# Optimization experiments

Measured on AMD Instinct MI355X. Metric: run time of the kernel, lower is better.

## Reference

```python
import jax, jax.numpy as jnp
import numpy as np

T = 8        # n_segment
T_OUT = 8    # t_out
G = 4        # n_group
K = 3        # correlation_neighbor


def setup_inputs() -> dict:
    key = jax.random.key(0)
    k1, k2, k3 = jax.random.split(key, 3)
    x = jax.random.normal(k1, (64, 256, 56, 56), dtype=jnp.float32)
    # grouped 1x1 conv: in=G*(T-1)*K*K=252 (63 per group), out=T_OUT*G*T=256 (64 per group)
    conv_w = jax.random.normal(k2, (G, T_OUT * T, (T - 1) * K * K), dtype=jnp.float32) * 0.05
    conv_b = jax.random.normal(k3, (G, T_OUT * T), dtype=jnp.float32) * 0.05
    return {"x": x, "conv_w": conv_w, "conv_b": conv_b}


def reference(x, conv_w, conv_b):
    nt, c, h, w = x.shape
    nb = nt // T
    cpg = c // G
    pad = K // 2

    x5 = x.reshape(nb, T, c, h, w)
    # ReplicationPad2d(pad) on spatial dims
    xp = jnp.pad(x5, ((0, 0), (0, 0), (0, 0), (pad, pad), (pad, pad)), mode='edge')

    # 9-way shifted cost volume: per-group channel-sum of x[t] * x_pad[t+1] shifted
    a = x5[:, :T - 1].reshape(nb, T - 1, G, cpg, h, w)
    corr_list = []
    for i in range(K):
        for j in range(K):
            b = xp[:, 1:, :, i:i + h, j:j + w].reshape(nb, T - 1, G, cpg, h, w)
            corr_list.append(jnp.einsum('ntgchw,ntgchw->ntghw', a, b))
    corr = jnp.stack(corr_list, axis=3)                     # (nb, T-1, G, K*K, h, w)
    corr = corr.transpose(0, 2, 1, 3, 4, 5)                 # (nb, G, T-1, K*K, h, w)
    corr = corr.reshape(nb, G, (T - 1) * K * K, h, w)

    # grouped 1x1 conv
    wx = jnp.einsum('ngihw,goi->ngohw', corr, conv_w) + conv_b[None, :, :, None, None]
    wx = wx.reshape(nb, G, T_OUT, T, h, w).transpose(2, 1, 0, 3, 4, 5)  # (t_out, G, nb, T, h, w)

    # torch splits c as (c_per_group, G) here (c_per_group outer) — mimic exactly
    xs = x5.reshape(nb, T, cpg, G, h, w).transpose(2, 3, 0, 1, 4, 5)   # (cpg, G, nb, T, h, w)

    # weighted segment-sum over T for each output frame
    xsum = jnp.einsum('ognthw,cgnthw->ocgnhw', wx, xs)      # (t_out, cpg, G, nb, h, w)

    # residual: x at frame floor(i*T/t_out)
    i_in = (np.arange(T_OUT) * T) // T_OUT
    res = xs[:, :, :, i_in].transpose(3, 0, 1, 2, 4, 5)     # (t_out, cpg, G, nb, h, w)

    out = (xsum + res).transpose(3, 0, 2, 1, 4, 5)          # (nb, t_out, G, cpg, h, w)
    return out.reshape(nb * T_OUT, c, h, w)
```

## Files before the change

kernel.cpp:

```cpp
#include <hip/hip_runtime.h>

namespace {
constexpr int NBb = 8;
constexpr int TT  = 8;
constexpr int TOo = 8;
constexpr int CC  = 256;
constexpr int GG  = 4;
constexpr int CPG = 64;
constexpr int HHH = 56;
constexpr int WWW = 56;
constexpr int HWs = HHH * WWW;
constexpr long CHW = (long)CC * HWs;
constexpr int NC  = (TT - 1) * 9;
}

__global__ __launch_bounds__(64, 2)
void corr_fusion(const float* __restrict__ x,
                 const float* __restrict__ conv_w,
                 const float* __restrict__ conv_b,
                 float* __restrict__ out)
{
    const int w  = threadIdx.x;
    const int wc = w < WWW - 1 ? w : WWW - 1;
    const int h  = blockIdx.x;
    const int g  = blockIdx.y;
    const int n  = blockIdx.z;
    const int hm = h > 0 ? h - 1 : 0;
    const int hp = h < HHH - 1 ? h + 1 : HHH - 1;

    const int offh = h  * WWW + wc;
    const int offm = hm * WWW + wc;
    const int offp = hp * WWW + wc;

    float corr[NC];
#pragma unroll
    for (int i = 0; i < NC; ++i) corr[i] = 0.0f;

    const float* xg = x + (long)n * TT * CHW + (long)g * CPG * HWs;

    for (int c = 0; c < CPG; ++c) {
        const float* xc = xg + (long)c * HWs;
        float rh[TT], rm[TT - 1], rp[TT - 1];
#pragma unroll
        for (int t = 0; t < TT; ++t) rh[t] = xc[(long)t * CHW + offh];
#pragma unroll
        for (int t = 1; t < TT; ++t) {
            rm[t - 1] = xc[(long)t * CHW + offm];
            rp[t - 1] = xc[(long)t * CHW + offp];
        }
#pragma unroll
        for (int t = 0; t < TT - 1; ++t) {
            const float a = rh[t];
#pragma unroll
            for (int di = 0; di < 3; ++di) {
                float bc = (di == 0) ? rm[t] : (di == 1) ? rh[t + 1] : rp[t];
                float bl = __shfl_up(bc, 1);
                if (w == 0) bl = bc;
                float br = __shfl_down(bc, 1);
                if (w == WWW - 1) br = bc;
                const int base = t * 9 + di * 3;
                corr[base + 0] = fmaf(a, bl, corr[base + 0]);
                corr[base + 1] = fmaf(a, bc, corr[base + 1]);
                corr[base + 2] = fmaf(a, br, corr[base + 2]);
            }
        }
    }

    const float* cw = conv_w + (long)g * (TOo * TT) * NC;
    const float* cb = conv_b + g * (TOo * TT);
    float wx[TOo * TT];
#pragma unroll
    for (int o = 0; o < TOo * TT; ++o) {
        float s = cb[o];
#pragma unroll
        for (int i = 0; i < NC; ++i) s = fmaf(cw[o * NC + i], corr[i], s);
        wx[o] = s;
    }

    const float* xn = x   + (long)n * TT  * CHW;
    float*       on = out + (long)n * TOo * CHW;
    for (int cp = 0; cp < CPG; ++cp) {
        const float* xc = xn + (long)(cp * GG + g) * HWs + offh;
        float xv[TT];
#pragma unroll
        for (int t = 0; t < TT; ++t) xv[t] = xc[(long)t * CHW];
        if (w < WWW) {
            float* oc = on + (long)(g * CPG + cp) * HWs + h * WWW + w;
#pragma unroll
            for (int to = 0; to < TOo; ++to) {
                float s = xv[to];
#pragma unroll
                for (int t = 0; t < TT; ++t) s = fmaf(wx[to * TT + t], xv[t], s);
                oc[(long)to * CHW] = s;
            }
        }
    }
}

extern "C" void kernel_launch(void* const* d_in, const int* in_sizes, int n_in,
                              void* d_out, int out_size, void* d_ws, size_t ws_size,
                              hipStream_t stream) {
    const float* x  = (const float*)d_in[0];
    const float* cw = (const float*)d_in[1];
    const float* cb = (const float*)d_in[2];
    float* out = (float*)d_out;

    dim3 grid(HHH, GG, NBb);
    dim3 block(64);
    hipLaunchKernelGGL(corr_fusion, grid, block, 0, stream, x, cw, cb, out);
}
```

Baseline: 483.8 us.

## Split channel loops across four waves per block with shared-memory reduction

Each block now runs four waves instead of one. Each wave accumulates the correlation over a quarter of the channels, and the partial sums are reduced with LDS atomics. The grouped 1x1 conv outputs are computed per wave (16 each) and shared through LDS. The output loop is also split across waves. This raises parallelism, since the grid had only 1792 single-wave blocks, and shortens each thread's serial channel loop. The cost is extra LDS traffic, barriers, and a launch bound of 256 threads with 4 blocks per CU, which may cause register spills given the large per-thread arrays.

```diff
diff --git a/kernel.cpp b/kernel.cpp
--- a/kernel.cpp
+++ b/kernel.cpp
@@ -12,16 +12,22 @@
 constexpr int HWs = HHH * WWW;
 constexpr long CHW = (long)CC * HWs;
 constexpr int NC  = (TT - 1) * 9;
+constexpr int NW  = 4;
+constexpr int CPW = CPG / NW;
 }
 
-__global__ __launch_bounds__(64, 2)
+__global__ __launch_bounds__(256, 4)
 void corr_fusion(const float* __restrict__ x,
                  const float* __restrict__ conv_w,
                  const float* __restrict__ conv_b,
                  float* __restrict__ out)
 {
-    const int w  = threadIdx.x;
-    const int wc = w < WWW - 1 ? w : WWW - 1;
+    __shared__ float smem[64][64];
+
+    const int tid  = threadIdx.x;
+    const int w    = tid & 63;
+    const int wave = tid >> 6;
+    const int wc   = w < WWW - 1 ? w : WWW - 1;
     const int h  = blockIdx.x;
     const int g  = blockIdx.y;
     const int n  = blockIdx.z;
@@ -32,13 +38,16 @@
     const int offm = hm * WWW + wc;
     const int offp = hp * WWW + wc;
 
+    for (int i = tid; i < NC * 64; i += 256) (&smem[0][0])[i] = 0.0f;
+    __syncthreads();
+
     float corr[NC];
 #pragma unroll
     for (int i = 0; i < NC; ++i) corr[i] = 0.0f;
 
     const float* xg = x + (long)n * TT * CHW + (long)g * CPG * HWs;
 
-    for (int c = 0; c < CPG; ++c) {
+    for (int c = wave * CPW; c < wave * CPW + CPW; ++c) {
         const float* xc = xg + (long)c * HWs;
         float rh[TT], rm[TT - 1], rp[TT - 1];
 #pragma unroll
@@ -66,20 +75,38 @@
         }
     }
 
+#pragma unroll
+    for (int i = 0; i < NC; ++i) atomicAdd(&smem[i][w], corr[i]);
+    __syncthreads();
+
+    float corr_r[NC];
+#pragma unroll
+    for (int i = 0; i < NC; ++i) corr_r[i] = smem[i][w];
+    __syncthreads();
+
     const float* cw = conv_w + (long)g * (TOo * TT) * NC;
     const float* cb = conv_b + g * (TOo * TT);
-    float wx[TOo * TT];
+    float wx16[CPW];
 #pragma unroll
-    for (int o = 0; o < TOo * TT; ++o) {
+    for (int oo = 0; oo < CPW; ++oo) {
+        const int o = wave * CPW + oo;
         float s = cb[o];
 #pragma unroll
-        for (int i = 0; i < NC; ++i) s = fmaf(cw[o * NC + i], corr[i], s);
-        wx[o] = s;
+        for (int i = 0; i < NC; ++i) s = fmaf(cw[o * NC + i], corr_r[i], s);
+        wx16[oo] = s;
     }
+#pragma unroll
+    for (int oo = 0; oo < CPW; ++oo) smem[wave * CPW + oo][w] = wx16[oo];
+    __syncthreads();
+
+    float wxr[TOo * TT];
+#pragma unroll
+    for (int o = 0; o < TOo * TT; ++o) wxr[o] = smem[o][w];
 
     const float* xn = x   + (long)n * TT  * CHW;
     float*       on = out + (long)n * TOo * CHW;
-    for (int cp = 0; cp < CPG; ++cp) {
+    for (int cpi = 0; cpi < CPW; ++cpi) {
+        const int cp = wave * CPW + cpi;
         const float* xc = xn + (long)(cp * GG + g) * HWs + offh;
         float xv[TT];
 #pragma unroll
@@ -90,7 +117,7 @@
             for (int to = 0; to < TOo; ++to) {
                 float s = xv[to];
 #pragma unroll
-                for (int t = 0; t < TT; ++t) s = fmaf(wx[to * TT + t], xv[t], s);
+                for (int t = 0; t < TT; ++t) s = fmaf(wxr[to * TT + t], xv[t], s);
                 oc[(long)to * CHW] = s;
             }
         }
@@ -106,6 +133,6 @@
     float* out = (float*)d_out;
 
     dim3 grid(HHH, GG, NBb);
-    dim3 block(64);
+    dim3 block(256);
     hipLaunchKernelGGL(corr_fusion, grid, block, 0, stream, x, cw, cb, out);
 }
```

Measured after the change: 534.8 us. 1.11x slower.

## Split correlation into separate high-parallelism kernel with workspace buffer

Applied to the files above, without the earlier changes.

Splits the fused kernel into two. A correlation kernel parallelises over the time step as well, giving 7x more blocks with small accumulators, and uses a remapped block order. A fusion kernel then reads the correlation volume from workspace and computes the 1x1 conv across 4 waves per block, sharing the results through LDS. The goal is to raise occupancy and parallelism over the original register-heavy 1792-block launch, at the cost of writing and re-reading the corr volume through global memory. It falls back to the monolithic kernel when the workspace is too small.

```diff
diff --git a/kernel.cpp b/kernel.cpp
--- a/kernel.cpp
+++ b/kernel.cpp
@@ -12,13 +12,121 @@
 constexpr int HWs = HHH * WWW;
 constexpr long CHW = (long)CC * HWs;
 constexpr int NC  = (TT - 1) * 9;
+constexpr long CORR_ELEMS = (long)NBb * GG * NC * HWs;
+}
+
+__global__ __launch_bounds__(64, 8)
+void corr_k(const float* __restrict__ x, float* __restrict__ corr)
+{
+    const int lid = blockIdx.x + 392 * (blockIdx.y + 4 * blockIdx.z);
+    const int wg  = (lid & 7) * 1568 + (lid >> 3);
+    const int bx  = wg % 392;
+    const int rem = wg / 392;
+    const int g   = rem & 3;
+    const int n   = rem >> 2;
+    const int t   = bx / HHH;
+    const int h   = bx % HHH;
+
+    const int w  = threadIdx.x;
+    const int wc = w < WWW - 1 ? w : WWW - 1;
+    const int hm = h > 0 ? h - 1 : 0;
+    const int hp = h < HHH - 1 ? h + 1 : HHH - 1;
+
+    const float* xa = x + (long)n * TT * CHW + (long)g * CPG * HWs + (long)t * CHW;
+    const float* xb = xa + CHW;
+    const int offh = h  * WWW + wc;
+    const int offm = hm * WWW + wc;
+    const int offp = hp * WWW + wc;
+
+    float acc[9];
+#pragma unroll
+    for (int k = 0; k < 9; ++k) acc[k] = 0.0f;
+
+#pragma unroll 4
+    for (int c = 0; c < CPG; ++c) {
+        const long co = (long)c * HWs;
+        const float a  = xa[co + offh];
+        const float bm = xb[co + offm];
+        const float bc = xb[co + offh];
+        const float bp = xb[co + offp];
+        float bml = __shfl_up(bm, 1), bmr = __shfl_down(bm, 1);
+        float bcl = __shfl_up(bc, 1), bcr = __shfl_down(bc, 1);
+        float bpl = __shfl_up(bp, 1), bpr = __shfl_down(bp, 1);
+        if (w == 0) { bml = bm; bcl = bc; bpl = bp; }
+        acc[0] = fmaf(a, bml, acc[0]); acc[1] = fmaf(a, bm, acc[1]); acc[2] = fmaf(a, bmr, acc[2]);
+        acc[3] = fmaf(a, bcl, acc[3]); acc[4] = fmaf(a, bc, acc[4]); acc[5] = fmaf(a, bcr, acc[5]);
+        acc[6] = fmaf(a, bpl, acc[6]); acc[7] = fmaf(a, bp, acc[7]); acc[8] = fmaf(a, bpr, acc[8]);
+    }
+
+    if (w < WWW) {
+        float* co = corr + ((((long)n * GG + g) * 7 + t) * 9) * HWs + h * WWW + w;
+#pragma unroll
+        for (int k = 0; k < 9; ++k) co[(long)k * HWs] = acc[k];
+    }
+}
+
+__global__ __launch_bounds__(256, 2)
+void fuse_k(const float* __restrict__ x, const float* __restrict__ corr,
+            const float* __restrict__ conv_w, const float* __restrict__ conv_b,
+            float* __restrict__ out)
+{
+    __shared__ float swx[64][64];
+
+    const int tid  = threadIdx.x;
+    const int w    = tid & 63;
+    const int wave = tid >> 6;
+    const int wc   = w < WWW - 1 ? w : WWW - 1;
+    const int h = blockIdx.x;
+    const int g = blockIdx.y;
+    const int n = blockIdx.z;
+
+    float cr[NC];
+    const float* cbase = corr + (((long)n * GG + g) * NC) * HWs + h * WWW;
+#pragma unroll
+    for (int i = 0; i < NC; ++i) cr[i] = cbase[(long)i * HWs + wc];
+
+    const float* cw = conv_w + (long)g * (TOo * TT) * NC;
+    const float* cb = conv_b + g * (TOo * TT);
+#pragma unroll
+    for (int oo = 0; oo < 16; ++oo) {
+        const int o = wave * 16 + oo;
+        float s = cb[o];
+#pragma unroll
+        for (int i = 0; i < NC; ++i) s = fmaf(cw[o * NC + i], cr[i], s);
+        swx[o][w] = s;
+    }
+    __syncthreads();
+
+    float wxr[TOo * TT];
+#pragma unroll
+    for (int o = 0; o < TOo * TT; ++o) wxr[o] = swx[o][w];
+
+    const float* xn = x   + (long)n * TT  * CHW;
+    float*       on = out + (long)n * TOo * CHW;
+    for (int cpi = 0; cpi < 16; ++cpi) {
+        const int cp = wave * 16 + cpi;
+        const float* xc = xn + (long)(cp * GG + g) * HWs + h * WWW + wc;
+        float xv[TT];
+#pragma unroll
+        for (int t = 0; t < TT; ++t) xv[t] = xc[(long)t * CHW];
+        if (w < WWW) {
+            float* oc = on + (long)(g * CPG + cp) * HWs + h * WWW + w;
+#pragma unroll
+            for (int to = 0; to < TOo; ++to) {
+                float s = xv[to];
+#pragma unroll
+                for (int t = 0; t < TT; ++t) s = fmaf(wxr[to * TT + t], xv[t], s);
+                oc[(long)to * CHW] = s;
+            }
+        }
+    }
 }
 
 __global__ __launch_bounds__(64, 2)
-void corr_fusion(const float* __restrict__ x,
-                 const float* __restrict__ conv_w,
-                 const float* __restrict__ conv_b,
-                 float* __restrict__ out)
+void corr_fusion_mono(const float* __restrict__ x,
+                      const float* __restrict__ conv_w,
+                      const float* __restrict__ conv_b,
+                      float* __restrict__ out)
 {
     const int w  = threadIdx.x;
     const int wc = w < WWW - 1 ? w : WWW - 1;
@@ -105,7 +213,14 @@
     const float* cb = (const float*)d_in[2];
     float* out = (float*)d_out;
 
-    dim3 grid(HHH, GG, NBb);
-    dim3 block(64);
-    hipLaunchKernelGGL(corr_fusion, grid, block, 0, stream, x, cw, cb, out);
-}
+    if (ws_size >= CORR_ELEMS * sizeof(float)) {
+        float* corr = (float*)d_ws;
+        dim3 gridA(7 * HHH, GG, NBb);
+        hipLaunchKernelGGL(corr_k, gridA, dim3(64), 0, stream, x, corr);
+        dim3 gridB(HHH, GG, NBb);
+        hipLaunchKernelGGL(fuse_k, gridB, dim3(256), 0, stream, x, corr, cw, cb, out);
+    } else {
+        dim3 grid(HHH, GG, NBb);
+        hipLaunchKernelGGL(corr_fusion_mono, grid, dim3(64), 0, stream, x, cw, cb, out);
+    }
+}
```

Result: slower. 516.7 us (+6.8%).

## Split fused kernel into corr, conv and segment-sum kernels via workspace

Applied to the files above, without the earlier changes.

Replaces the single fused kernel, which had only 1792 blocks holding large register arrays, with three kernels. The first computes the cost volume per (n,g,t) over two rows. The second applies the grouped 1x1 conv over flat 64-pixel tiles. The third does the weighted segment-sum, with an XCD-aware block index remap. The aim is more parallelism and occupancy and less register pressure, paid for with extra workspace traffic for the corr and wx intermediates. The old fused kernel remains as a fallback when the workspace is too small.

```diff
diff --git a/kernel.cpp b/kernel.cpp
--- a/kernel.cpp
+++ b/kernel.cpp
@@ -4,21 +4,154 @@
 constexpr int NBb = 8;
 constexpr int TT  = 8;
 constexpr int TOo = 8;
-constexpr int CC  = 256;
 constexpr int GG  = 4;
 constexpr int CPG = 64;
 constexpr int HHH = 56;
 constexpr int WWW = 56;
 constexpr int HWs = HHH * WWW;
-constexpr long CHW = (long)CC * HWs;
+constexpr long CHW = (long)256 * HWs;
 constexpr int NC  = (TT - 1) * 9;
+constexpr long CORR_ELEMS = (long)NBb * GG * NC * HWs;
+constexpr long WX_ELEMS   = (long)NBb * GG * (TOo * TT) * HWs;
+}
+
+__global__ __launch_bounds__(64, 6)
+void corr2_k(const float* __restrict__ x, float* __restrict__ corr)
+{
+    const int lid = blockIdx.x + 196 * (blockIdx.y + 4 * blockIdx.z);
+    const int wg  = (lid & 7) * 784 + (lid >> 3);
+    int r  = wg;
+    const int hb = r % 28; r /= 28;
+    const int t  = r % 7;  r /= 7;
+    const int g  = r % 4;  r /= 4;
+    const int n  = r;
+
+    const int h0 = hb * 2, h1 = h0 + 1;
+    const int w  = threadIdx.x;
+    const int wc = w < WWW - 1 ? w : WWW - 1;
+    const int rm = h0 > 0 ? h0 - 1 : 0;
+    const int rp = h1 < HHH - 1 ? h1 + 1 : HHH - 1;
+
+    const float* xa = x + (long)n * TT * CHW + (long)g * CPG * HWs + (long)t * CHW;
+    const float* xb = xa + CHW;
+    const int o0 = h0 * WWW + wc, o1 = h1 * WWW + wc;
+    const int om = rm * WWW + wc, op = rp * WWW + wc;
+
+    float accA[9], accB[9];
+#pragma unroll
+    for (int k = 0; k < 9; ++k) { accA[k] = 0.0f; accB[k] = 0.0f; }
+
+#pragma unroll 4
+    for (int c = 0; c < CPG; ++c) {
+        const long co = (long)c * HWs;
+        const float a0 = xa[co + o0];
+        const float a1 = xa[co + o1];
+        const float r0 = xb[co + om];
+        const float r1 = xb[co + o0];
+        const float r2 = xb[co + o1];
+        const float r3 = xb[co + op];
+        float r0l = __shfl_up(r0, 1), r0r = __shfl_down(r0, 1);
+        float r1l = __shfl_up(r1, 1), r1r = __shfl_down(r1, 1);
+        float r2l = __shfl_up(r2, 1), r2r = __shfl_down(r2, 1);
+        float r3l = __shfl_up(r3, 1), r3r = __shfl_down(r3, 1);
+        if (w == 0) { r0l = r0; r1l = r1; r2l = r2; r3l = r3; }
+        accA[0] = fmaf(a0, r0l, accA[0]); accA[1] = fmaf(a0, r0, accA[1]); accA[2] = fmaf(a0, r0r, accA[2]);
+        accA[3] = fmaf(a0, r1l, accA[3]); accA[4] = fmaf(a0, r1, accA[4]); accA[5] = fmaf(a0, r1r, accA[5]);
+        accA[6] = fmaf(a0, r2l, accA[6]); accA[7] = fmaf(a0, r2, accA[7]); accA[8] = fmaf(a0, r2r, accA[8]);
+        accB[0] = fmaf(a1, r1l, accB[0]); accB[1] = fmaf(a1, r1, accB[1]); accB[2] = fmaf(a1, r1r, accB[2]);
+        accB[3] = fmaf(a1, r2l, accB[3]); accB[4] = fmaf(a1, r2, accB[4]); accB[5] = fmaf(a1, r2r, accB[5]);
+        accB[6] = fmaf(a1, r3l, accB[6]); accB[7] = fmaf(a1, r3, accB[7]); accB[8] = fmaf(a1, r3r, accB[8]);
+    }
+
+    if (w < WWW) {
+        float* co = corr + ((((long)n * GG + g) * 7 + t) * 9) * HWs + w;
+#pragma unroll
+        for (int k = 0; k < 9; ++k) {
+            co[(long)k * HWs + h0 * WWW] = accA[k];
+            co[(long)k * HWs + h1 * WWW] = accB[k];
+        }
+    }
+}
+
+__global__ __launch_bounds__(64, 4)
+void conv_k(const float* __restrict__ corr,
+            const float* __restrict__ conv_w, const float* __restrict__ conv_b,
+            float* __restrict__ wxws)
+{
+    const int lid = blockIdx.x + 49 * (blockIdx.y + 16 * blockIdx.z);
+    const int wg  = (lid & 7) * 784 + (lid >> 3);
+    int r = wg;
+    const int och = r % 4;  r /= 4;
+    const int bx  = r % 49; r /= 49;
+    const int g   = r % 4;  r /= 4;
+    const int n   = r;
+
+    const int pix = bx * 64 + threadIdx.x;
+
+    const float* cbase = corr + (((long)n * GG + g) * NC) * HWs + pix;
+    float cr[NC];
+#pragma unroll
+    for (int i = 0; i < NC; ++i) cr[i] = cbase[(long)i * HWs];
+
+    const float* cw = conv_w + (long)g * (TOo * TT) * NC;
+    const float* cb = conv_b + g * (TOo * TT);
+    float* wbase = wxws + (((long)n * GG + g) * (TOo * TT)) * HWs + pix;
+
+#pragma unroll
+    for (int oo = 0; oo < 16; ++oo) {
+        const int o = och * 16 + oo;
+        float s = cb[o];
+#pragma unroll
+        for (int i = 0; i < NC; ++i) s = fmaf(cw[o * NC + i], cr[i], s);
+        wbase[(long)o * HWs] = s;
+    }
+}
+
+__global__ __launch_bounds__(64, 4)
+void seg_k(const float* __restrict__ x, const float* __restrict__ wxws,
+           float* __restrict__ out)
+{
+    const int lid = blockIdx.x + 49 * (blockIdx.y + 32 * blockIdx.z);
+    const int wg  = (lid & 7) * 1568 + (lid >> 3);
+    int r = wg;
+    const int cch = r % 8;  r /= 8;
+    const int bx  = r % 49; r /= 49;
+    const int g   = r % 4;  r /= 4;
+    const int n   = r;
+
+    const int pix = bx * 64 + threadIdx.x;
+
+    const float* wbase = wxws + (((long)n * GG + g) * (TOo * TT)) * HWs + pix;
+    float wxr[TOo * TT];
+#pragma unroll
+    for (int o = 0; o < TOo * TT; ++o) wxr[o] = wbase[(long)o * HWs];
+
+    const float* xn = x   + (long)n * TT  * CHW;
+    float*       on = out + (long)n * TOo * CHW;
+
+#pragma unroll
+    for (int cpi = 0; cpi < 8; ++cpi) {
+        const int cp = cch * 8 + cpi;
+        const float* xc = xn + (long)(cp * GG + g) * HWs + pix;
+        float xv[TT];
+#pragma unroll
+        for (int t = 0; t < TT; ++t) xv[t] = xc[(long)t * CHW];
+        float* oc = on + (long)(g * CPG + cp) * HWs + pix;
+#pragma unroll
+        for (int to = 0; to < TOo; ++to) {
+            float s = xv[to];
+#pragma unroll
+            for (int t = 0; t < TT; ++t) s = fmaf(wxr[to * TT + t], xv[t], s);
+            oc[(long)to * CHW] = s;
+        }
+    }
 }
 
 __global__ __launch_bounds__(64, 2)
-void corr_fusion(const float* __restrict__ x,
-                 const float* __restrict__ conv_w,
-                 const float* __restrict__ conv_b,
-                 float* __restrict__ out)
+void corr_fusion_mono(const float* __restrict__ x,
+                      const float* __restrict__ conv_w,
+                      const float* __restrict__ conv_b,
+                      float* __restrict__ out)
 {
     const int w  = threadIdx.x;
     const int wc = w < WWW - 1 ? w : WWW - 1;
@@ -105,7 +238,17 @@
     const float* cb = (const float*)d_in[2];
     float* out = (float*)d_out;
 
-    dim3 grid(HHH, GG, NBb);
-    dim3 block(64);
-    hipLaunchKernelGGL(corr_fusion, grid, block, 0, stream, x, cw, cb, out);
-}
+    if (ws_size >= (CORR_ELEMS + WX_ELEMS) * sizeof(float)) {
+        float* corr = (float*)d_ws;
+        float* wxws = corr + CORR_ELEMS;
+        dim3 gridA(196, GG, NBb);
+        hipLaunchKernelGGL(corr2_k, gridA, dim3(64), 0, stream, x, corr);
+        dim3 gridC(49, GG * 4, NBb);
+        hipLaunchKernelGGL(conv_k, gridC, dim3(64), 0, stream, corr, cw, cb, wxws);
+        dim3 gridS(49, GG * 8, NBb);
+        hipLaunchKernelGGL(seg_k, gridS, dim3(64), 0, stream, x, wxws, out);
+    } else {
+        dim3 grid(HHH, GG, NBb);
+        hipLaunchKernelGGL(corr_fusion_mono, grid, dim3(64), 0, stream, x, cw, cb, out);
+    }
+}
```

Measured after the change: 458.7 us. 1.05x faster.
